# Kernel tuning notes

Measured on AMD Instinct MI355X. Metric: run time of the kernel, lower is better.

## Reference

```python
import jax, jax.numpy as jnp
import numpy as np

B, S, D = 4, 4096, 256


def setup_inputs() -> dict:
    key = jax.random.key(0)
    ks = jax.random.split(key, 7)
    s = 1.0 / np.sqrt(D)
    return {
        "x": jax.random.normal(ks[0], (B, S, D), dtype=jnp.float32),
        "Wq": jax.random.normal(ks[1], (D, D), dtype=jnp.float32) * s,
        "bq": jax.random.normal(ks[2], (D,), dtype=jnp.float32) * s,
        "Wk": jax.random.normal(ks[3], (D, D), dtype=jnp.float32) * s,
        "bk": jax.random.normal(ks[4], (D,), dtype=jnp.float32) * s,
        "Wv": jax.random.normal(ks[5], (D, D), dtype=jnp.float32) * s,
        "bv": jax.random.normal(ks[6], (D,), dtype=jnp.float32) * s,
    }


def reference(x, Wq, bq, Wk, bk, Wv, bv):
    # QKV projections (torch Linear: y = x @ W^T + b; here W stored as [in, out])
    Q = jax.nn.relu(jnp.einsum("bsd,df->bsf", x, Wq) + bq)  # [B,S,D]
    K = jax.nn.relu(jnp.einsum("bsd,df->bsf", x, Wk) + bk)  # [B,S,D]
    V = jnp.einsum("bsd,df->bsf", x, Wv) + bv               # [B,S,D]
    scores = jnp.einsum("bqd,bkd->bqk", Q, K)               # [B,S,S], no 1/sqrt(d) scaling (as in source)
    attn = jax.nn.softmax(scores, axis=-1)
    return jnp.einsum("bqk,bkd->bqd", attn, V)              # [B,S,D]
```

## Files before the change

kernel.cpp:

```cpp
#include <hip/hip_runtime.h>
#include <stdint.h>

typedef __bf16 bf16;
typedef bf16 bf16x8 __attribute__((ext_vector_type(8)));
typedef _Float16 f16;
typedef f16 f16x8 __attribute__((ext_vector_type(8)));
typedef f16 f16x4 __attribute__((ext_vector_type(4)));
typedef float f32x4 __attribute__((ext_vector_type(4)));
typedef float f32x16 __attribute__((ext_vector_type(16)));
typedef unsigned short u16;
typedef unsigned int u32;
typedef u32 u32x2 __attribute__((ext_vector_type(2)));
typedef u16 u16x8v __attribute__((ext_vector_type(8)));

#define LOG2E 1.44269504088896340736f

__device__ __forceinline__ u16 f2bf(float f) {
  u32 u = __float_as_uint(f);
  u32 r = u + 0x7fffu + ((u >> 16) & 1u);
  return (u16)(r >> 16);
}
__device__ __forceinline__ float bf2f(u16 h) { return __uint_as_float(((u32)h) << 16); }

__device__ __forceinline__ u32 pkrtz(float a, float b) {
  auto r = __builtin_amdgcn_cvt_pkrtz(a, b);
  u32 u; __builtin_memcpy(&u, &r, 4);
  return u;
}
__device__ __forceinline__ float xmax32(float v) {
  u32x2 r = __builtin_amdgcn_permlane32_swap(__float_as_uint(v), __float_as_uint(v), false, false);
  return fmaxf(__uint_as_float(r[0]), __uint_as_float(r[1]));
}
__device__ __forceinline__ float xsum32(float v) {
  u32x2 r = __builtin_amdgcn_permlane32_swap(__float_as_uint(v), __float_as_uint(v), false, false);
  return __uint_as_float(r[0]) + __uint_as_float(r[1]);
}

union ABu { u16x8v u; bf16x8 b; };
union PAu { u32 w[4]; f16x8 v; };

__global__ void wt_kernel(const float* __restrict__ Wq, const float* __restrict__ Wk,
                          const float* __restrict__ Wv, u16* __restrict__ Wh,
                          u16* __restrict__ Wl) {
  int w = blockIdx.x >> 4;
  int chunk = blockIdx.x & 15;
  const float* W = (w == 0) ? Wq : (w == 1) ? Wk : Wv;
  int t = threadIdx.x;
  int o = chunk * 16 + (t & 15);
  int i0 = (t >> 4) * 16;
  u16x8v h0, h1, l0, l1;
  #pragma unroll
  for (int ii = 0; ii < 8; ++ii) {
    float v0 = W[(size_t)(i0 + ii) * 256 + o];
    u16 h = f2bf(v0); h0[ii] = h; l0[ii] = f2bf(v0 - bf2f(h));
    float v1 = W[(size_t)(i0 + 8 + ii) * 256 + o];
    h = f2bf(v1); h1[ii] = h; l1[ii] = f2bf(v1 - bf2f(h));
  }
  size_t base = (size_t)w * 65536 + (size_t)o * 256 + i0;
  *(u16x8v*)(Wh + base) = h0; *(u16x8v*)(Wh + base + 8) = h1;
  *(u16x8v*)(Wl + base) = l0; *(u16x8v*)(Wl + base + 8) = l1;
}

__global__ __launch_bounds__(256, 2) void proj_kernel(
    const float* __restrict__ x, const float* __restrict__ bq,
    const float* __restrict__ bk, const float* __restrict__ bv,
    const u16* __restrict__ Wh, const u16* __restrict__ Wl,
    f16* __restrict__ Qf, f16* __restrict__ Kf, f16* __restrict__ Vt) {
  __shared__ __align__(16) char Whs[16384];
  __shared__ __align__(16) char Wls[16384];

  int m = blockIdx.x, w = blockIdx.y;
  int tid = threadIdx.x, lane = tid & 63, wv = tid >> 6;
  int r = lane & 15, c = lane >> 4;
  int row0 = m * 128 + wv * 32;
  const char* Whw = (const char*)(Wh + (size_t)w * 65536);
  const char* Wlw = (const char*)(Wl + (size_t)w * 65536);
  const float* bias = (w == 0) ? bq : (w == 1) ? bk : bv;

  f32x4 acc[2][16];
  #pragma unroll
  for (int g = 0; g < 2; ++g)
    #pragma unroll
    for (int n = 0; n < 16; ++n) acc[g][n] = (f32x4)0.0f;

  for (int ks = 0; ks < 8; ++ks) {
    if (ks) __syncthreads();
    #pragma unroll
    for (int ss = 0; ss < 4; ++ss) {
      int slot = ss * 256 + tid;
      int row = slot >> 2, c4 = slot & 3;
      int dby = (c4 << 4) ^ (((row >> 1) & 3) << 4);
      const char* gh = Whw + (size_t)row * 512 + ks * 64 + dby;
      const char* gl = Wlw + (size_t)row * 512 + ks * 64 + dby;
      __builtin_amdgcn_global_load_lds(
          (const __attribute__((address_space(1))) void*)gh,
          (__attribute__((address_space(3))) void*)(Whs + slot * 16), 16, 0, 0);
      __builtin_amdgcn_global_load_lds(
          (const __attribute__((address_space(1))) void*)gl,
          (__attribute__((address_space(3))) void*)(Wls + slot * 16), 16, 0, 0);
    }
    __syncthreads();

    ABu ah[2], al[2];
    #pragma unroll
    for (int g = 0; g < 2; ++g) {
      const float* xrow = x + (size_t)(row0 + g * 16 + r) * 256 + ks * 32 + c * 8;
      float4 a0 = *(const float4*)(xrow);
      float4 a1 = *(const float4*)(xrow + 4);
      float xv[8] = {a0.x, a0.y, a0.z, a0.w, a1.x, a1.y, a1.z, a1.w};
      #pragma unroll
      for (int j = 0; j < 8; ++j) {
        u16 h = f2bf(xv[j]);
        ah[g].u[j] = h;
        al[g].u[j] = f2bf(xv[j] - bf2f(h));
      }
    }
    #pragma unroll
    for (int n = 0; n < 16; ++n) {
      int wrow = n * 16 + r;
      int wof = (c * 16) ^ (((wrow >> 1) & 3) << 4);
      bf16x8 whf = *(const bf16x8*)(Whs + wrow * 64 + wof);
      bf16x8 wlf = *(const bf16x8*)(Wls + wrow * 64 + wof);
      #pragma unroll
      for (int g = 0; g < 2; ++g) {
        acc[g][n] = __builtin_amdgcn_mfma_f32_16x16x32_bf16(ah[g].b, whf, acc[g][n], 0, 0, 0);
        acc[g][n] = __builtin_amdgcn_mfma_f32_16x16x32_bf16(al[g].b, whf, acc[g][n], 0, 0, 0);
        acc[g][n] = __builtin_amdgcn_mfma_f32_16x16x32_bf16(ah[g].b, wlf, acc[g][n], 0, 0, 0);
      }
    }
  }

  if (w < 2) {
    f16* outp = (w == 0) ? Qf : Kf;
    float osc = (w == 0) ? LOG2E : 1.0f;
    #pragma unroll
    for (int g = 0; g < 2; ++g)
      #pragma unroll
      for (int n = 0; n < 16; ++n) {
        int col = n * 16 + r;
        float bb = bias[col];
        #pragma unroll
        for (int i = 0; i < 4; ++i) {
          float v = fmaxf(acc[g][n][i] + bb, 0.0f) * osc;
          outp[(size_t)(row0 + g * 16 + c * 4 + i) * 256 + col] = (f16)v;
        }
      }
  } else {
    #pragma unroll
    for (int g = 0; g < 2; ++g) {
      int grow = row0 + g * 16 + c * 4;
      int b = grow >> 12, s0 = grow & 4095;
      #pragma unroll
      for (int n = 0; n < 16; ++n) {
        int d = n * 16 + r;
        float bb = bias[d];
        f16x4 pk;
        #pragma unroll
        for (int i = 0; i < 4; ++i) pk[i] = (f16)(acc[g][n][i] + bb);
        *(f16x4*)(Vt + (size_t)(b * 256 + d) * 4096 + s0) = pk;
      }
    }
  }
}

__global__ __launch_bounds__(512, 2) void attn_kernel(
    const f16* __restrict__ Qf, const f16* __restrict__ Kf,
    const f16* __restrict__ Vt, f16* __restrict__ Opart, float* __restrict__ Ml) {
  __shared__ __align__(16) char Ksm[2][32768];
  __shared__ __align__(16) char Vsm[2][32768];

  int bid = blockIdx.x;
  int xcd = bid & 7;
  int batch = xcd >> 1;
  int kq = ((xcd & 1) << 1) | ((bid >> 3) & 1);
  int qtl = bid >> 4;
  int tid = threadIdx.x, lane = tid & 63, wv = tid >> 6;
  int ln = lane & 31, hi = lane >> 5;
  int q0 = qtl * 256 + wv * 32;
  int kv0 = kq * 1024;
  int par = wv & 1;

  f16x8 qf[16];
  {
    const f16* qp = Qf + ((size_t)(batch * 4096 + q0 + ln)) * 256 + hi * 8;
    #pragma unroll
    for (int ks = 0; ks < 16; ++ks) qf[ks] = *(const f16x8*)(qp + ks * 16);
  }

  f32x16 O[8];
  #pragma unroll
  for (int dt = 0; dt < 8; ++dt) O[dt] = (f32x16)0.0f;
  float m_ = -1.0e30f, l_ = 0.0f;

  const char* Kbase = (const char*)(Kf + ((size_t)(batch * 4096 + kv0)) * 256);
  const char* Vbase = (const char*)(Vt + (size_t)batch * 1048576 + kv0);

#define STAGE(T, BF)                                                           \
  {                                                                            \
    _Pragma("unroll")                                                          \
    for (int rr = 0; rr < 4; ++rr) {                                           \
      int slot = rr * 512 + tid;                                               \
      int krow = slot >> 5;                                                    \
      int dby = ((slot & 31) << 4) ^ ((krow & 7) << 4);                        \
      const char* g = Kbase + (size_t)((T) * 64 + krow) * 512 + dby;           \
      __builtin_amdgcn_global_load_lds(                                        \
          (const __attribute__((address_space(1))) void*)g,                    \
          (__attribute__((address_space(3))) void*)(Ksm[BF] + slot * 16), 16, 0, 0); \
    }                                                                          \
    _Pragma("unroll")                                                          \
    for (int rr = 0; rr < 4; ++rr) {                                           \
      int slot = rr * 512 + tid;                                               \
      int vrow = slot >> 3;                                                    \
      int dby = ((slot & 7) << 4) ^ ((vrow & 7) << 4);                         \
      const char* g = Vbase + (size_t)vrow * 8192 + (T) * 128 + dby;           \
      __builtin_amdgcn_global_load_lds(                                        \
          (const __attribute__((address_space(1))) void*)g,                    \
          (__attribute__((address_space(3))) void*)(Vsm[BF] + slot * 16), 16, 0, 0); \
    }                                                                          \
  }

  int kswz = (ln & 7) << 4;
  int vswz = (ln & 7) << 4;
  int hi16 = hi * 16;
  int kbA = par * 32;
  int kbB = 32 - kbA;

#define SOFTMAX(SA, PA0, PA1)                                                  \
  {                                                                            \
    float pm = fmaxf(                                                          \
        fmaxf(fmaxf(fmaxf(SA[0], SA[1]), fmaxf(SA[2], SA[3])),                 \
              fmaxf(fmaxf(SA[4], SA[5]), fmaxf(SA[6], SA[7]))),                \
        fmaxf(fmaxf(fmaxf(SA[8], SA[9]), fmaxf(SA[10], SA[11])),               \
              fmaxf(fmaxf(SA[12], SA[13]), fmaxf(SA[14], SA[15]))));           \
    pm = xmax32(pm);                                                           \
    if (!__all(pm <= m_ + 11.5416f)) {       \
      float mn = fmaxf(m_, pm);                                                \
      float sc = exp2f(m_ - mn);                                               \
      m_ = mn; l_ *= sc;                                                       \
      _Pragma("unroll")                                                        \
      for (int rg = 0; rg < 16; ++rg) {                                        \
        float srg = __shfl(sc, (rg & 3) + 8 * (rg >> 2) + 4 * hi);             \
        _Pragma("unroll")                                                      \
        for (int dt = 0; dt < 8; ++dt) O[dt][rg] *= srg;                       \
      }                                                                        \
    }                                                                          \
    float p_[16];                                                              \
    _Pragma("unroll")                                                          \
    for (int j = 0; j < 16; ++j) p_[j] = exp2f(SA[j] - m_);                    \
    float ps = (((p_[0] + p_[1]) + (p_[2] + p_[3])) +                          \
                ((p_[4] + p_[5]) + (p_[6] + p_[7]))) +                         \
               (((p_[8] + p_[9]) + (p_[10] + p_[11])) +                        \
                ((p_[12] + p_[13]) + (p_[14] + p_[15])));                      \
    l_ += xsum32(ps);                                                          \
    {                                                                          \
      u32x2 r1 = __builtin_amdgcn_permlane32_swap(pkrtz(p_[0], p_[1]), pkrtz(p_[4], p_[5]), false, false); \
      u32x2 r2 = __builtin_amdgcn_permlane32_swap(pkrtz(p_[2], p_[3]), pkrtz(p_[6], p_[7]), false, false); \
      PA0.w[0] = r1[0]; PA0.w[1] = r2[0]; PA0.w[2] = r1[1]; PA0.w[3] = r2[1];  \
      u32x2 r3 = __builtin_amdgcn_permlane32_swap(pkrtz(p_[8], p_[9]), pkrtz(p_[12], p_[13]), false, false); \
      u32x2 r4 = __builtin_amdgcn_permlane32_swap(pkrtz(p_[10], p_[11]), pkrtz(p_[14], p_[15]), false, false); \
      PA1.w[0] = r3[0]; PA1.w[1] = r4[0]; PA1.w[2] = r3[1]; PA1.w[3] = r4[1];  \
    }                                                                          \
  }

  STAGE(0, 0);

  for (int t = 0; t < 16; ++t) {
    __builtin_amdgcn_s_barrier();
    if (t < 15) {
      STAGE(t + 1, (t + 1) & 1);
      asm volatile("s_waitcnt vmcnt(8)" ::: "memory");
    } else {
      asm volatile("s_waitcnt vmcnt(0)" ::: "memory");
    }
    __builtin_amdgcn_sched_barrier(0);
    __builtin_amdgcn_s_barrier();

    const char* Kc = Ksm[t & 1];
    const char* Vc = Vsm[t & 1];
    const char* KcA = Kc + kbA * 512;
    const char* KcB = Kc + kbB * 512;
    int vbA = kbA * 2, vbB = kbB * 2;

    f32x16 sA = (f32x16)0.0f;
    __builtin_amdgcn_s_setprio(1);
    #pragma unroll
    for (int ks = 0; ks < 16; ++ks) {
      f16x8 kf = *(const f16x8*)(KcA + ln * 512 + ((ks * 32 + hi16) ^ kswz));
      sA = __builtin_amdgcn_mfma_f32_32x32x16_f16(kf, qf[ks], sA, 0, 0, 0);
    }
    __builtin_amdgcn_s_setprio(0);
    PAu paA0, paA1;
    SOFTMAX(sA, paA0, paA1);

    f32x16 sB = (f32x16)0.0f;
    __builtin_amdgcn_s_setprio(1);
    #pragma unroll
    for (int ks = 0; ks < 16; ++ks) {
      f16x8 kf = *(const f16x8*)(KcB + ln * 512 + ((ks * 32 + hi16) ^ kswz));
      sB = __builtin_amdgcn_mfma_f32_32x32x16_f16(kf, qf[ks], sB, 0, 0, 0);
      int dt = ks >> 1, k2 = ks & 1;
      f16x8 vf = *(const f16x8*)(Vc + (dt * 32 + ln) * 128 + ((vbA + k2 * 32 + hi16) ^ vswz));
      O[dt] = __builtin_amdgcn_mfma_f32_32x32x16_f16(k2 ? paA1.v : paA0.v, vf, O[dt], 0, 0, 0);
    }
    __builtin_amdgcn_s_setprio(0);
    PAu paB0, paB1;
    SOFTMAX(sB, paB0, paB1);

    __builtin_amdgcn_s_setprio(1);
    #pragma unroll
    for (int ks = 0; ks < 16; ++ks) {
      int dt = ks >> 1, k2 = ks & 1;
      f16x8 vf = *(const f16x8*)(Vc + (dt * 32 + ln) * 128 + ((vbB + k2 * 32 + hi16) ^ vswz));
      O[dt] = __builtin_amdgcn_mfma_f32_32x32x16_f16(k2 ? paB1.v : paB0.v, vf, O[dt], 0, 0, 0);
    }
    __builtin_amdgcn_s_setprio(0);
  }

  float invl = 1.0f / l_;
  #pragma unroll
  for (int rg = 0; rg < 16; ++rg) {
    int qr = (rg & 3) + 8 * (rg >> 2) + 4 * hi;
    float iv = __shfl(invl, qr);
    size_t row = (size_t)kq * 16384 + batch * 4096 + q0 + qr;
    #pragma unroll
    for (int dt = 0; dt < 8; ++dt)
      Opart[row * 256 + dt * 32 + ln] = (f16)(O[dt][rg] * iv);
  }
  if (hi == 0) {
    size_t grow = (size_t)kq * 16384 + batch * 4096 + q0 + ln;
    Ml[grow * 2] = m_;
    Ml[grow * 2 + 1] = l_;
  }
#undef STAGE
#undef SOFTMAX
}

__global__ __launch_bounds__(256) void merge_kernel(
    const f16* __restrict__ Opart, const float* __restrict__ Ml,
    float* __restrict__ out) {
  int gid = blockIdx.x * 256 + threadIdx.x;
  int row = gid >> 5, d0 = (gid & 31) * 8;
  float m[4], l[4];
  #pragma unroll
  for (int p = 0; p < 4; ++p) {
    m[p] = Ml[((size_t)p * 16384 + row) * 2];
    l[p] = Ml[((size_t)p * 16384 + row) * 2 + 1];
  }
  float M = fmaxf(fmaxf(m[0], m[1]), fmaxf(m[2], m[3]));
  float wl[4], L = 0.f;
  #pragma unroll
  for (int p = 0; p < 4; ++p) { wl[p] = exp2f(m[p] - M) * l[p]; L += wl[p]; }
  float o[8] = {0.f, 0.f, 0.f, 0.f, 0.f, 0.f, 0.f, 0.f};
  #pragma unroll
  for (int p = 0; p < 4; ++p) {
    f16x8 v = *(const f16x8*)(Opart + ((size_t)p * 16384 + row) * 256 + d0);
    #pragma unroll
    for (int j = 0; j < 8; ++j) o[j] += wl[p] * (float)v[j];
  }
  float invL = 1.0f / L;
  float4 o0 = {o[0] * invL, o[1] * invL, o[2] * invL, o[3] * invL};
  float4 o1 = {o[4] * invL, o[5] * invL, o[6] * invL, o[7] * invL};
  *(float4*)(out + (size_t)row * 256 + d0) = o0;
  *(float4*)(out + (size_t)row * 256 + d0 + 4) = o1;
}

extern "C" void kernel_launch(void* const* d_in, const int* in_sizes, int n_in,
                              void* d_out, int out_size, void* d_ws, size_t ws_size,
                              hipStream_t stream) {
  const float* x  = (const float*)d_in[0];
  const float* Wq = (const float*)d_in[1];
  const float* bq = (const float*)d_in[2];
  const float* Wk = (const float*)d_in[3];
  const float* bk = (const float*)d_in[4];
  const float* Wv = (const float*)d_in[5];
  const float* bv = (const float*)d_in[6];
  float* out = (float*)d_out;

  u16* Wh = (u16*)d_ws;
  u16* Wl = Wh + 3 * 65536;
  f16* Qf = (f16*)(Wl + 3 * 65536);
  f16* Kf = Qf + (size_t)16384 * 256;
  f16* Vt = Kf + (size_t)16384 * 256;
  f16* Opart = Vt + (size_t)4 * 256 * 4096;
  float* Ml = (float*)(Opart + (size_t)4 * 16384 * 256);

  wt_kernel<<<48, 256, 0, stream>>>(Wq, Wk, Wv, Wh, Wl);
  proj_kernel<<<dim3(128, 3), 256, 0, stream>>>(x, bq, bk, bv, Wh, Wl, Qf, Kf, Vt);
  attn_kernel<<<256, 512, 0, stream>>>(Qf, Kf, Vt, Opart, Ml);
  merge_kernel<<<2048, 256, 0, stream>>>(Opart, Ml, out);
}
```

Before: 153.8 us.

## Interleave softmax with QK and PV MFMAs and peel first KV tile

Restructures the attention inner loop so the row-max and exp computation for one 32-key half is interleaved between the MFMAs of the next QK product and the current PV product, hiding VALU softmax work behind matrix instructions. The per-wave parity ordering of key halves is dropped so every wave processes halves in the same order. The first tile is peeled so it can initialize the running max directly instead of starting from a sentinel, and the rescale step is applied to already-exponentiated values after the fact. This raises register pressure and relies on the compiler preserving the hand-interleaved order. Dropping the parity alternation may increase LDS bank contention between waves.

Measured after the change: 194.9 us. +26.7%, slower.

```diff
diff --git a/kernel.cpp b/kernel.cpp
--- a/kernel.cpp
+++ b/kernel.cpp
@@ -178,7 +178,6 @@
   int ln = lane & 31, hi = lane >> 5;
   int q0 = qtl * 256 + wv * 32;
   int kv0 = kq * 1024;
-  int par = wv & 1;
 
   f16x8 qf[16];
   {
@@ -190,7 +189,7 @@
   f32x16 O[8];
   #pragma unroll
   for (int dt = 0; dt < 8; ++dt) O[dt] = (f32x16)0.0f;
-  float m_ = -1.0e30f, l_ = 0.0f;
+  float m_ = 0.0f, l_ = 0.0f;
 
   const char* Kbase = (const char*)(Kf + ((size_t)(batch * 4096 + kv0)) * 256);
   const char* Vbase = (const char*)(Vt + (size_t)batch * 1048576 + kv0);
@@ -222,49 +221,103 @@
   int kswz = (ln & 7) << 4;
   int vswz = (ln & 7) << 4;
   int hi16 = hi * 16;
-  int kbA = par * 32;
-  int kbB = 32 - kbA;
-
-#define SOFTMAX(SA, PA0, PA1)                                                  \
-  {                                                                            \
-    float pm = fmaxf(                                                          \
-        fmaxf(fmaxf(fmaxf(SA[0], SA[1]), fmaxf(SA[2], SA[3])),                 \
-              fmaxf(fmaxf(SA[4], SA[5]), fmaxf(SA[6], SA[7]))),                \
-        fmaxf(fmaxf(fmaxf(SA[8], SA[9]), fmaxf(SA[10], SA[11])),               \
-              fmaxf(fmaxf(SA[12], SA[13]), fmaxf(SA[14], SA[15]))));           \
-    pm = xmax32(pm);                                                           \
-    if (!__all(pm <= m_ + 11.5416f)) {       \
-      float mn = fmaxf(m_, pm);                                                \
-      float sc = exp2f(m_ - mn);                                               \
-      m_ = mn; l_ *= sc;                                                       \
+
+#define QKS(SACC, KO, ks)                                                      \
+  { f16x8 kf = *(const f16x8*)(Kc + ((KO) + ln) * 512 + (((ks) * 32 + hi16) ^ kswz)); \
+    SACC = __builtin_amdgcn_mfma_f32_32x32x16_f16(kf, qf[ks], SACC, 0, 0, 0); }
+#define PVS(PA, dt, VO)                                                        \
+  { f16x8 vf = *(const f16x8*)(Vc + ((dt) * 32 + ln) * 128 + (((VO) + hi16) ^ vswz)); \
+    O[dt] = __builtin_amdgcn_mfma_f32_32x32x16_f16(PA, vf, O[dt], 0, 0, 0); }
+#define ROWMAX(S, PM)                                                          \
+  float PM;                                                                    \
+  { float z0 = fmaxf(fmaxf(S[0], S[1]), fmaxf(S[2], S[3]));                    \
+    float z1 = fmaxf(fmaxf(S[4], S[5]), fmaxf(S[6], S[7]));                    \
+    float z2 = fmaxf(fmaxf(S[8], S[9]), fmaxf(S[10], S[11]));                  \
+    float z3 = fmaxf(fmaxf(S[12], S[13]), fmaxf(S[14], S[15]));                \
+    PM = xmax32(fmaxf(fmaxf(z0, z1), fmaxf(z2, z3))); }
+#define SM_EXP(S, j0, PS)                                                      \
+  { S[j0] = exp2f(S[j0] - m_); S[(j0)+1] = exp2f(S[(j0)+1] - m_);              \
+    S[(j0)+2] = exp2f(S[(j0)+2] - m_); S[(j0)+3] = exp2f(S[(j0)+3] - m_);      \
+    PS += ((S[j0] + S[(j0)+1]) + (S[(j0)+2] + S[(j0)+3])); }
+#define P2FRAG(S, PA0, PA1)                                                    \
+  { u32x2 r1 = __builtin_amdgcn_permlane32_swap(pkrtz(S[0], S[1]), pkrtz(S[4], S[5]), false, false); \
+    u32x2 r2 = __builtin_amdgcn_permlane32_swap(pkrtz(S[2], S[3]), pkrtz(S[6], S[7]), false, false); \
+    PA0.w[0] = r1[0]; PA0.w[1] = r2[0]; PA0.w[2] = r1[1]; PA0.w[3] = r2[1];    \
+    u32x2 r3 = __builtin_amdgcn_permlane32_swap(pkrtz(S[8], S[9]), pkrtz(S[12], S[13]), false, false); \
+    u32x2 r4 = __builtin_amdgcn_permlane32_swap(pkrtz(S[10], S[11]), pkrtz(S[14], S[15]), false, false); \
+    PA1.w[0] = r3[0]; PA1.w[1] = r4[0]; PA1.w[2] = r3[1]; PA1.w[3] = r4[1]; }
+#define SM_FINISH(S, PM, PS, PA0, PA1)                                         \
+  if (!__all((PM) <= m_ + 11.5416f)) {                                         \
+    float mn = fmaxf(m_, (PM));                                                \
+    float sc = exp2f(m_ - mn);                                                 \
+    m_ = mn; l_ *= sc; (PS) *= sc;                                             \
+    _Pragma("unroll")                                                          \
+    for (int j = 0; j < 16; ++j) S[j] *= sc;                                   \
+    _Pragma("unroll")                                                          \
+    for (int rg = 0; rg < 16; ++rg) {                                          \
+      float srg = __shfl(sc, (rg & 3) + 8 * (rg >> 2) + 4 * hi);               \
       _Pragma("unroll")                                                        \
-      for (int rg = 0; rg < 16; ++rg) {                                        \
-        float srg = __shfl(sc, (rg & 3) + 8 * (rg >> 2) + 4 * hi);             \
-        _Pragma("unroll")                                                      \
-        for (int dt = 0; dt < 8; ++dt) O[dt][rg] *= srg;                       \
-      }                                                                        \
+      for (int dt = 0; dt < 8; ++dt) O[dt][rg] *= srg;                         \
     }                                                                          \
-    float p_[16];                                                              \
-    _Pragma("unroll")                                                          \
-    for (int j = 0; j < 16; ++j) p_[j] = exp2f(SA[j] - m_);                    \
-    float ps = (((p_[0] + p_[1]) + (p_[2] + p_[3])) +                          \
-                ((p_[4] + p_[5]) + (p_[6] + p_[7]))) +                         \
-               (((p_[8] + p_[9]) + (p_[10] + p_[11])) +                        \
-                ((p_[12] + p_[13]) + (p_[14] + p_[15])));                      \
-    l_ += xsum32(ps);                                                          \
-    {                                                                          \
-      u32x2 r1 = __builtin_amdgcn_permlane32_swap(pkrtz(p_[0], p_[1]), pkrtz(p_[4], p_[5]), false, false); \
-      u32x2 r2 = __builtin_amdgcn_permlane32_swap(pkrtz(p_[2], p_[3]), pkrtz(p_[6], p_[7]), false, false); \
-      PA0.w[0] = r1[0]; PA0.w[1] = r2[0]; PA0.w[2] = r1[1]; PA0.w[3] = r2[1];  \
-      u32x2 r3 = __builtin_amdgcn_permlane32_swap(pkrtz(p_[8], p_[9]), pkrtz(p_[12], p_[13]), false, false); \
-      u32x2 r4 = __builtin_amdgcn_permlane32_swap(pkrtz(p_[10], p_[11]), pkrtz(p_[14], p_[15]), false, false); \
-      PA1.w[0] = r3[0]; PA1.w[1] = r4[0]; PA1.w[2] = r3[1]; PA1.w[3] = r4[1];  \
-    }                                                                          \
-  }
+  }                                                                            \
+  l_ += xsum32(PS);                                                            \
+  P2FRAG(S, PA0, PA1)
 
   STAGE(0, 0);
 
-  for (int t = 0; t < 16; ++t) {
+  {
+    __builtin_amdgcn_s_barrier();
+    STAGE(1, 1);
+    asm volatile("s_waitcnt vmcnt(8)" ::: "memory");
+    __builtin_amdgcn_sched_barrier(0);
+    __builtin_amdgcn_s_barrier();
+
+    const char* Kc = Ksm[0];
+    const char* Vc = Vsm[0];
+
+    f32x16 sAa = (f32x16)0.0f;
+    f32x16 sAb = (f32x16)0.0f;
+    __builtin_amdgcn_s_setprio(1);
+    #pragma unroll
+    for (int ks = 0; ks < 16; ++ks) QKS(sAa, 0, ks);
+    #pragma unroll
+    for (int ks = 0; ks < 16; ++ks) QKS(sAb, 32, ks);
+    __builtin_amdgcn_s_setprio(0);
+
+    ROWMAX(sAa, pmA);
+    m_ = pmA;
+    float psA = 0.0f;
+    SM_EXP(sAa, 0, psA); SM_EXP(sAa, 4, psA);
+    SM_EXP(sAa, 8, psA); SM_EXP(sAa, 12, psA);
+    l_ = xsum32(psA);
+    PAu paA0, paA1;
+    P2FRAG(sAa, paA0, paA1);
+
+    __builtin_amdgcn_s_setprio(1);
+    #pragma unroll
+    for (int ks = 0; ks < 16; ++ks) {
+      int dt = ks >> 1, k2 = ks & 1;
+      PVS(k2 ? paA1.v : paA0.v, dt, k2 * 32);
+    }
+    __builtin_amdgcn_s_setprio(0);
+
+    ROWMAX(sAb, pmB);
+    float psB = 0.0f;
+    SM_EXP(sAb, 0, psB); SM_EXP(sAb, 4, psB);
+    SM_EXP(sAb, 8, psB); SM_EXP(sAb, 12, psB);
+    PAu paB0, paB1;
+    SM_FINISH(sAb, pmB, psB, paB0, paB1);
+
+    __builtin_amdgcn_s_setprio(1);
+    #pragma unroll
+    for (int ks = 0; ks < 16; ++ks) {
+      int dt = ks >> 1, k2 = ks & 1;
+      PVS(k2 ? paB1.v : paB0.v, dt, 64 + k2 * 32);
+    }
+    __builtin_amdgcn_s_setprio(0);
+  }
+
+  for (int t = 1; t < 16; ++t) {
     __builtin_amdgcn_s_barrier();
     if (t < 15) {
       STAGE(t + 1, (t + 1) & 1);
@@ -277,41 +330,74 @@
 
     const char* Kc = Ksm[t & 1];
     const char* Vc = Vsm[t & 1];
-    const char* KcA = Kc + kbA * 512;
-    const char* KcB = Kc + kbB * 512;
-    int vbA = kbA * 2, vbB = kbB * 2;
-
-    f32x16 sA = (f32x16)0.0f;
-    __builtin_amdgcn_s_setprio(1);
-    #pragma unroll
-    for (int ks = 0; ks < 16; ++ks) {
-      f16x8 kf = *(const f16x8*)(KcA + ln * 512 + ((ks * 32 + hi16) ^ kswz));
-      sA = __builtin_amdgcn_mfma_f32_32x32x16_f16(kf, qf[ks], sA, 0, 0, 0);
-    }
+
+    f32x16 sAa = (f32x16)0.0f;
+    __builtin_amdgcn_s_setprio(1);
+    #pragma unroll
+    for (int ks = 0; ks < 16; ++ks) QKS(sAa, 0, ks);
+
+    f32x16 sAb = (f32x16)0.0f;
+    float psA = 0.0f;
+    QKS(sAb, 32, 0); QKS(sAb, 32, 1);
+    float a0 = fmaxf(sAa[0], sAa[1]), a1 = fmaxf(sAa[2], sAa[3]);
+    QKS(sAb, 32, 2); QKS(sAb, 32, 3);
+    float a2 = fmaxf(sAa[4], sAa[5]), a3 = fmaxf(sAa[6], sAa[7]);
+    QKS(sAb, 32, 4); QKS(sAb, 32, 5);
+    float a4 = fmaxf(sAa[8], sAa[9]), a5 = fmaxf(sAa[10], sAa[11]);
+    QKS(sAb, 32, 6); QKS(sAb, 32, 7);
+    float a6 = fmaxf(sAa[12], sAa[13]), a7 = fmaxf(sAa[14], sAa[15]);
+    QKS(sAb, 32, 8);
+    a0 = fmaxf(fmaxf(a0, a1), fmaxf(a2, a3));
+    QKS(sAb, 32, 9);
+    a4 = fmaxf(fmaxf(a4, a5), fmaxf(a6, a7));
+    QKS(sAb, 32, 10);
+    float pmA = xmax32(fmaxf(a0, a4));
+    QKS(sAb, 32, 11);
+    SM_EXP(sAa, 0, psA);
+    QKS(sAb, 32, 12);
+    SM_EXP(sAa, 4, psA);
+    QKS(sAb, 32, 13);
+    SM_EXP(sAa, 8, psA);
+    QKS(sAb, 32, 14);
+    SM_EXP(sAa, 12, psA);
+    QKS(sAb, 32, 15);
     __builtin_amdgcn_s_setprio(0);
     PAu paA0, paA1;
-    SOFTMAX(sA, paA0, paA1);
-
-    f32x16 sB = (f32x16)0.0f;
-    __builtin_amdgcn_s_setprio(1);
-    #pragma unroll
-    for (int ks = 0; ks < 16; ++ks) {
-      f16x8 kf = *(const f16x8*)(KcB + ln * 512 + ((ks * 32 + hi16) ^ kswz));
-      sB = __builtin_amdgcn_mfma_f32_32x32x16_f16(kf, qf[ks], sB, 0, 0, 0);
-      int dt = ks >> 1, k2 = ks & 1;
-      f16x8 vf = *(const f16x8*)(Vc + (dt * 32 + ln) * 128 + ((vbA + k2 * 32 + hi16) ^ vswz));
-      O[dt] = __builtin_amdgcn_mfma_f32_32x32x16_f16(k2 ? paA1.v : paA0.v, vf, O[dt], 0, 0, 0);
-    }
+    SM_FINISH(sAa, pmA, psA, paA0, paA1);
+
+    float psB = 0.0f;
+    __builtin_amdgcn_s_setprio(1);
+    PVS(paA0.v, 0, 0); PVS(paA1.v, 0, 32);
+    float b0 = fmaxf(sAb[0], sAb[1]), b1 = fmaxf(sAb[2], sAb[3]);
+    PVS(paA0.v, 1, 0); PVS(paA1.v, 1, 32);
+    float b2 = fmaxf(sAb[4], sAb[5]), b3 = fmaxf(sAb[6], sAb[7]);
+    PVS(paA0.v, 2, 0); PVS(paA1.v, 2, 32);
+    float b4 = fmaxf(sAb[8], sAb[9]), b5 = fmaxf(sAb[10], sAb[11]);
+    PVS(paA0.v, 3, 0); PVS(paA1.v, 3, 32);
+    float b6 = fmaxf(sAb[12], sAb[13]), b7 = fmaxf(sAb[14], sAb[15]);
+    PVS(paA0.v, 4, 0); PVS(paA1.v, 4, 32);
+    b0 = fmaxf(fmaxf(b0, b1), fmaxf(b2, b3));
+    b4 = fmaxf(fmaxf(b4, b5), fmaxf(b6, b7));
+    PVS(paA0.v, 5, 0);
+    float pmB = xmax32(fmaxf(b0, b4));
+    PVS(paA1.v, 5, 32);
+    SM_EXP(sAb, 0, psB);
+    PVS(paA0.v, 6, 0);
+    SM_EXP(sAb, 4, psB);
+    PVS(paA1.v, 6, 32);
+    SM_EXP(sAb, 8, psB);
+    PVS(paA0.v, 7, 0);
+    SM_EXP(sAb, 12, psB);
+    PVS(paA1.v, 7, 32);
     __builtin_amdgcn_s_setprio(0);
     PAu paB0, paB1;
-    SOFTMAX(sB, paB0, paB1);
+    SM_FINISH(sAb, pmB, psB, paB0, paB1);
 
     __builtin_amdgcn_s_setprio(1);
     #pragma unroll
     for (int ks = 0; ks < 16; ++ks) {
       int dt = ks >> 1, k2 = ks & 1;
-      f16x8 vf = *(const f16x8*)(Vc + (dt * 32 + ln) * 128 + ((vbB + k2 * 32 + hi16) ^ vswz));
-      O[dt] = __builtin_amdgcn_mfma_f32_32x32x16_f16(k2 ? paB1.v : paB0.v, vf, O[dt], 0, 0, 0);
+      PVS(k2 ? paB1.v : paB0.v, dt, 64 + k2 * 32);
     }
     __builtin_amdgcn_s_setprio(0);
   }
@@ -332,7 +418,12 @@
     Ml[grow * 2 + 1] = l_;
   }
 #undef STAGE
-#undef SOFTMAX
+#undef QKS
+#undef PVS
+#undef ROWMAX
+#undef SM_EXP
+#undef P2FRAG
+#undef SM_FINISH
 }
 
 __global__ __launch_bounds__(256) void merge_kernel(
```
